# Performance work log

Hardware: AMD Instinct MI355X
Metric: run time of the kernel (lower is better)

## Reference

```python
import jax, jax.numpy as jnp
import numpy as np

T, B, S, E, H = 64, 64, 128, 512, 1024  # tgt_len, batch, src_len, emb, hidden


def setup_inputs() -> dict:
    key = jax.random.key(0)
    ks = jax.random.split(key, 14)
    s = 0.02  # weight init scale
    f32 = jnp.float32
    return {
        "inp": jax.random.normal(ks[0], (T, B, E), f32),
        "context": jax.random.normal(ks[1], (S, B, H), f32),
        "h0": jax.random.normal(ks[2], (2, B, H), f32) * 0.1,
        "c0": jax.random.normal(ks[3], (2, B, H), f32) * 0.1,
        # layer 0 LSTMCell: input = emb + input-feed = E + H
        "W_ih0": jax.random.normal(ks[4], (4 * H, E + H), f32) * s,
        "b_ih0": jnp.zeros((4 * H,), f32),
        "W_hh0": jax.random.normal(ks[5], (4 * H, H), f32) * s,
        "b_hh0": jnp.zeros((4 * H,), f32),
        # layer 1 LSTMCell: input = H
        "W_ih1": jax.random.normal(ks[6], (4 * H, H), f32) * s,
        "b_ih1": jnp.zeros((4 * H,), f32),
        "W_hh1": jax.random.normal(ks[7], (4 * H, H), f32) * s,
        "b_hh1": jnp.zeros((4 * H,), f32),
        # global attention (general): linear_in W_a (H,H), linear_out (H, 2H) no bias
        "W_a": jax.random.normal(ks[8], (H, H), f32) * s,
        "W_out": jax.random.normal(ks[9], (H, 2 * H), f32) * s,
    }


def _lstm_cell(x, h, c, W_ih, b_ih, W_hh, b_hh):
    # PyTorch gate order: i, f, g, o
    g = x @ W_ih.T + b_ih + h @ W_hh.T + b_hh
    i, f, gg, o = jnp.split(g, 4, axis=-1)
    c2 = jax.nn.sigmoid(f) * c + jax.nn.sigmoid(i) * jnp.tanh(gg)
    h2 = jax.nn.sigmoid(o) * jnp.tanh(c2)
    return h2, c2


def reference(inp, context, h0, c0, W_ih0, b_ih0, W_hh0, b_hh0,
              W_ih1, b_ih1, W_hh1, b_hh1, W_a, W_out):
    ctx_bt = jnp.transpose(context, (1, 0, 2))          # (B, S, H)
    # score(h, s) = h . (ctx_s @ W_a)  (== (h @ W_a.T) . ctx_s)
    ctx_p = jnp.einsum('bsk,kd->bsd', ctx_bt, W_a)      # (B, S, H)

    def step(carry, emb_t):
        h, c, out = carry                                # h,c: (2,B,H); out: (B,H)
        x = jnp.concatenate([emb_t, out], axis=1)        # (B, E+H) input feed
        h0n, c0n = _lstm_cell(x, h[0], c[0], W_ih0, b_ih0, W_hh0, b_hh0)
        h1n, c1n = _lstm_cell(h0n, h[1], c[1], W_ih1, b_ih1, W_hh1, b_hh1)
        score = jnp.einsum('bh,bsh->bs', h1n, ctx_p)     # (B, S)
        align = jax.nn.softmax(score, axis=-1)
        cvec = jnp.einsum('bs,bsh->bh', align, ctx_bt)   # (B, H)
        attn_h = jnp.tanh(jnp.concatenate([cvec, h1n], axis=1) @ W_out.T)
        hn = jnp.stack([h0n, h1n])
        cn = jnp.stack([c0n, c1n])
        return (hn, cn, attn_h), (attn_h, align)

    out0 = jnp.zeros((context.shape[1], W_a.shape[0]), context.dtype)
    (hF, cF, _), (outs, attns) = jax.lax.scan(step, (h0, c0, out0), inp)
    # outs: (T, B, H); hF, cF: (2, B, H); attns: (T, B, S)
    return outs, hF, cF, attns
```

## Files before the change

### kernel.cpp

```cpp
#include <hip/hip_runtime.h>

#define T_ 64
#define B_ 64
#define S_ 128
#define E_ 512
#define H_ 1024
#define BH (B_ * H_)

#define W0ROW (E_ + 2 * H_ + 8)
#define W1ROW (2 * H_ + 8)
#define SMEM_BYTES ((16 * W0ROW + 16 * W1ROW) * 2)

typedef __attribute__((ext_vector_type(8))) short short8;
typedef __attribute__((ext_vector_type(4))) short short4v;
typedef __attribute__((ext_vector_type(4))) float f32x4;

static __device__ __forceinline__ float bf2f(ushort u) {
  union { float f; unsigned u; } x; x.u = ((unsigned)u) << 16; return x.f;
}
static __device__ __forceinline__ ushort f2bf(float f) {
  union { float f; unsigned u; } x; x.f = f;
  unsigned r = 0x7FFFu + ((x.u >> 16) & 1u);
  return (ushort)((x.u + r) >> 16);
}
static __device__ __forceinline__ float sigm(float x) {
  return 1.f / (1.f + expf(-x));
}

static __device__ __forceinline__ void st32_dev(unsigned* p, unsigned v) {
  __hip_atomic_store(p, v, __ATOMIC_RELAXED, __HIP_MEMORY_SCOPE_AGENT);
}
static __device__ __forceinline__ unsigned ld32_dev(const unsigned* p) {
  return __hip_atomic_load(p, __ATOMIC_RELAXED, __HIP_MEMORY_SCOPE_AGENT);
}
static __device__ __forceinline__ void stf_dev(float* p, float v) {
  union { float f; unsigned u; } x; x.f = v;
  st32_dev((unsigned*)p, x.u);
}

__global__ __launch_bounds__(256) void k_cvt(const float* __restrict__ src,
                                             ushort* __restrict__ dst, int n4) {
  int i = blockIdx.x * 256 + threadIdx.x;
  if (i >= n4) return;
  f32x4 v = ((const f32x4*)src)[i];
  short4v o;
  o[0] = (short)f2bf(v[0]); o[1] = (short)f2bf(v[1]);
  o[2] = (short)f2bf(v[2]); o[3] = (short)f2bf(v[3]);
  ((short4v*)dst)[i] = o;
}

__global__ __launch_bounds__(256) void k_cvtT(const float* __restrict__ src,
                                              ushort* __restrict__ dst) {
  __shared__ ushort tile[32][33];
  const int bx = blockIdx.x & 31;
  const int by = blockIdx.x >> 5;
  const int lx = threadIdx.x & 31, ly = threadIdx.x >> 5;
#pragma unroll
  for (int i = 0; i < 32; i += 8)
    tile[ly + i][lx] = f2bf(src[(size_t)(by * 32 + ly + i) * H_ + bx * 32 + lx]);
  __syncthreads();
#pragma unroll
  for (int i = 0; i < 32; i += 8)
    dst[(size_t)(bx * 32 + ly + i) * H_ + by * 32 + lx] = tile[lx][ly + i];
}

__global__ __launch_bounds__(256) void k_ctxp(const ushort* __restrict__ ctx,
                                              const ushort* __restrict__ WaT,
                                              ushort* __restrict__ ctxp) {
  const int tid = threadIdx.x;
  const int wave = tid >> 6, lane = tid & 63;
  const int quad = lane >> 4, l16 = lane & 15;
  const int m0 = blockIdx.x * 64 + wave * 16;
  const int n0 = blockIdx.y * 64;
  const ushort* ar = ctx + (size_t)(m0 + l16) * H_;
  const int koff = quad * 8;
  f32x4 acc[4] = {};
  for (int k0 = 0; k0 < H_; k0 += 32) {
    int kk = k0 + koff;
    short8 a = *(const short8*)(ar + kk);
#pragma unroll
    for (int nt = 0; nt < 4; ++nt) {
      short8 b = *(const short8*)(WaT + (size_t)(n0 + nt * 16 + l16) * H_ + kk);
      acc[nt] = __builtin_amdgcn_mfma_f32_16x16x32_bf16(a, b, acc[nt], 0, 0, 0);
    }
  }
#pragma unroll
  for (int nt = 0; nt < 4; ++nt)
#pragma unroll
    for (int r = 0; r < 4; ++r)
      ctxp[(size_t)(m0 + quad * 4 + r) * H_ + n0 + nt * 16 + l16] =
          f2bf(acc[nt][r]);
}

__global__ __launch_bounds__(256) void k_init(const float* __restrict__ h0in,
                                              ushort* __restrict__ h0b,
                                              ushort* __restrict__ h1b,
                                              ushort* __restrict__ fdb,
                                              unsigned* __restrict__ flags) {
  int i = blockIdx.x * 256 + threadIdx.x;
  h0b[i] = f2bf(h0in[i]);
  h1b[i] = f2bf(h0in[BH + i]);
  fdb[i] = 0;
  if (blockIdx.x == 0) flags[threadIdx.x * 16] = 0;
}

static __device__ __forceinline__ void grid_bar(unsigned* flags, unsigned gen) {
  __syncthreads();
  if (blockIdx.x == 0) {
    const int tid = threadIdx.x;
    if (tid > 0 && tid < 256) {
      while (ld32_dev(&flags[tid * 16]) < gen) __builtin_amdgcn_s_sleep(4);
    }
    __syncthreads();
    if (tid == 0) st32_dev(&flags[0], gen);
    __syncthreads();
  } else {
    if (threadIdx.x == 0) {
      st32_dev(&flags[blockIdx.x * 16], gen);
      while (ld32_dev(&flags[0]) < gen) __builtin_amdgcn_s_sleep(4);
    }
    __syncthreads();
  }
  asm volatile("" ::: "memory");
}

struct FusedP {
  const ushort* inp;
  const ushort* Wih0; const ushort* Whh0;
  const ushort* Wih1; const ushort* Whh1;
  const ushort* Wout;
  const ushort* ctx;
  const ushort* ctxp;
  const float* bih0; const float* bhh0;
  const float* bih1; const float* bhh1;
  const float* c0in;
  ushort* h0b;
  ushort* h1b;
  ushort* fdb;
  ushort* cvb;
  float* psb;
  float* outs; float* hF; float* cF; float* attns;
  unsigned* flags;
};

#define ST(w, r, c) ub[(w) * 272 + (r) * 17 + (c)]
#define RED(w, i)   ub[(w) * 256 + (i)]

__global__ __launch_bounds__(1024, 1) void k_fused(FusedP p) {
  extern __shared__ ushort wlds[];
  ushort* w0 = wlds;
  ushort* w1 = wlds + 16 * W0ROW;
  __shared__ float ub[2176];
  __shared__ float al[S_];
  const int blk = blockIdx.x;
  const int tid = threadIdx.x;
  const int wave = tid >> 6, lane = tid & 63;
  const int wg = wave & 3;
  const int kh = wave >> 2;
  const int quad = lane >> 4, l16 = lane & 15;
  const int j0 = blk * 4;

  for (int idx = tid; idx < 16 * 192; idx += 1024) {
    int r = idx / 192, c = (idx % 192) * 8;
    int n = (r >> 2) * H_ + j0 + (r & 3);
    *(short8*)(w0 + r * W0ROW + c) =
        *(const short8*)(p.Wih0 + (size_t)n * (E_ + H_) + c);
  }
  for (int idx = tid; idx < 16 * 128; idx += 1024) {
    int r = idx / 128, c = (idx % 128) * 8;
    int n = (r >> 2) * H_ + j0 + (r & 3);
    *(short8*)(w0 + r * W0ROW + (E_ + H_) + c) =
        *(const short8*)(p.Whh0 + (size_t)n * H_ + c);
  }
  for (int idx = tid; idx < 16 * 128; idx += 1024) {
    int r = idx / 128, c = (idx % 128) * 8;
    int n = (r >> 2) * H_ + j0 + (r & 3);
    *(short8*)(w1 + r * W1ROW + c) =
        *(const short8*)(p.Wih1 + (size_t)n * H_ + c);
  }
  for (int idx = tid; idx < 16 * 128; idx += 1024) {
    int r = idx / 128, c = (idx % 128) * 8;
    int n = (r >> 2) * H_ + j0 + (r & 3);
    *(short8*)(w1 + r * W1ROW + H_ + c) =
        *(const short8*)(p.Whh1 + (size_t)n * H_ + c);
  }
  __syncthreads();

  const int own_b = tid >> 2;
  const int own_jl = tid & 3;
  const int own_j = j0 + own_jl;
  const int own_idx = own_b * H_ + own_j;
  float c0reg = 0.f, c1reg = 0.f;
  float b0i = 0.f, b0f = 0.f, b0g = 0.f, b0o = 0.f;
  float b1i = 0.f, b1f = 0.f, b1g = 0.f, b1o = 0.f;
  if (tid < 256) {
    c0reg = p.c0in[own_idx];
    c1reg = p.c0in[BH + own_idx];
    b0i = p.bih0[own_j]          + p.bhh0[own_j];
    b0f = p.bih0[H_ + own_j]     + p.bhh0[H_ + own_j];
    b0g = p.bih0[2 * H_ + own_j] + p.bhh0[2 * H_ + own_j];
    b0o = p.bih0[3 * H_ + own_j] + p.bhh0[3 * H_ + own_j];
    b1i = p.bih1[own_j]          + p.bhh1[own_j];
    b1f = p.bih1[H_ + own_j]     + p.bhh1[H_ + own_j];
    b1g = p.bih1[2 * H_ + own_j] + p.bhh1[2 * H_ + own_j];
    b1o = p.bih1[3 * H_ + own_j] + p.bhh1[3 * H_ + own_j];
  }

  const ushort* w0r = w0 + l16 * W0ROW;
  const ushort* w1r = w1 + l16 * W1ROW;
  const int koff = quad * 8;

  const int b3 = blk >> 2, dq = blk & 3;
  const int d0 = dq * 256;

  unsigned gen = 0;

  for (int t = 0; t < T_; ++t) {
    const ushort* h0prev = p.h0b + (size_t)t * BH;
    ushort* h0new       = p.h0b + (size_t)(t + 1) * BH;
    const ushort* h1prev = p.h1b + (size_t)t * BH;
    ushort* h1new       = p.h1b + (size_t)(t + 1) * BH;
    const ushort* feedr  = p.fdb + (size_t)t * BH;
    ushort* feedw       = p.fdb + (size_t)(t + 1) * BH;
    ushort* cv          = p.cvb + (size_t)t * BH;
    float* pst          = p.psb + (size_t)t * B_ * S_ * 4;
    const int last = (t == T_ - 1);

    {
      const int arow = 16 * wg + l16;
      const ushort* er = p.inp + ((size_t)t * B_ + arow) * E_;
      const ushort* fr = feedr + (size_t)arow * H_;
      const ushort* hr = h0prev + (size_t)arow * H_;
      const int kbase = kh * 640;
      f32x4 acc = {};
#pragma unroll
      for (int k0 = 0; k0 < 640; k0 += 32) {
        int kk = kbase + k0 + koff;
        short8 a;
        if (kk < E_)            a = *(const short8*)(er + kk);
        else if (kk < E_ + H_)  a = *(const short8*)(fr + (kk - E_));
        else                    a = *(const short8*)(hr + (kk - E_ - H_));
        short8 b = *(const short8*)(w0r + kk);
        acc = __builtin_amdgcn_mfma_f32_16x16x32_bf16(a, b, acc, 0, 0, 0);
      }
      if (kh >= 2) {
#pragma unroll
        for (int r = 0; r < 4; ++r) ST(wave - 8, quad * 4 + r, l16) = acc[r];
      }
      __syncthreads();
      if (kh < 2) {
#pragma unroll
        for (int r = 0; r < 4; ++r) {
          float s = ST(wave, quad * 4 + r, l16) + acc[r];
          ST(wave, quad * 4 + r, l16) = s;
        }
      }
      __syncthreads();
      if (tid < 256) {
        const int w = own_b >> 4, bl = own_b & 15;
        float gi = ST(w, bl, 0 + own_jl)  + ST(w + 4, bl, 0 + own_jl)  + b0i;
        float gf = ST(w, bl, 4 + own_jl)  + ST(w + 4, bl, 4 + own_jl)  + b0f;
        float gg = ST(w, bl, 8 + own_jl)  + ST(w + 4, bl, 8 + own_jl)  + b0g;
        float go = ST(w, bl, 12 + own_jl) + ST(w + 4, bl, 12 + own_jl) + b0o;
        float cn = sigm(gf) * c0reg + sigm(gi) * tanhf(gg);
        float hn = sigm(go) * tanhf(cn);
        c0reg = cn;
        if (last) { p.hF[own_idx] = hn; p.cF[own_idx] = cn; }
        unsigned u = f2bf(hn);
        unsigned up = __shfl_down(u, 1);
        if (!(own_jl & 1))
          st32_dev((unsigned*)h0new + own_b * (H_ / 2) + blk * 2 + (own_jl >> 1),
                   u | (up << 16));
      }
    }
    grid_bar(p.flags, ++gen);

    {
      const int arow = 16 * wg + l16;
      const ushort* xr = h0new + (size_t)arow * H_;
      const ushort* hr = h1prev + (size_t)arow * H_;
      const int kbase = kh * 512;
      f32x4 acc = {};
#pragma unroll
      for (int k0 = 0; k0 < 512; k0 += 32) {
        int kk = kbase + k0 + koff;
        short8 a = (kk < H_) ? *(const short8*)(xr + kk)
                             : *(const short8*)(hr + (kk - H_));
        short8 b = *(const short8*)(w1r + kk);
        acc = __builtin_amdgcn_mfma_f32_16x16x32_bf16(a, b, acc, 0, 0, 0);
      }
      if (kh >= 2) {
#pragma unroll
        for (int r = 0; r < 4; ++r) ST(wave - 8, quad * 4 + r, l16) = acc[r];
      }
      __syncthreads();
      if (kh < 2) {
#pragma unroll
        for (int r = 0; r < 4; ++r) {
          float s = ST(wave, quad * 4 + r, l16) + acc[r];
          ST(wave, quad * 4 + r, l16) = s;
        }
      }
      __syncthreads();
      if (tid < 256) {
        const int w = own_b >> 4, bl = own_b & 15;
        float gi = ST(w, bl, 0 + own_jl)  + ST(w + 4, bl, 0 + own_jl)  + b1i;
        float gf = ST(w, bl, 4 + own_jl)  + ST(w + 4, bl, 4 + own_jl)  + b1f;
        float gg = ST(w, bl, 8 + own_jl)  + ST(w + 4, bl, 8 + own_jl)  + b1g;
        float go = ST(w, bl, 12 + own_jl) + ST(w + 4, bl, 12 + own_jl) + b1o;
        float cn = sigm(gf) * c1reg + sigm(gi) * tanhf(gg);
        float hn = sigm(go) * tanhf(cn);
        c1reg = cn;
        if (last) { p.hF[BH + own_idx] = hn; p.cF[BH + own_idx] = cn; }
        unsigned u = f2bf(hn);
        unsigned up = __shfl_down(u, 1);
        if (!(own_jl & 1))
          st32_dev((unsigned*)h1new + own_b * (H_ / 2) + blk * 2 + (own_jl >> 1),
                   u | (up << 16));
      }
    }
    grid_bar(p.flags, ++gen);

    {
      short4v qv = *(const short4v*)(h1new + (size_t)b3 * H_ + d0 + lane * 4);
      float q0 = bf2f((ushort)qv[0]), q1 = bf2f((ushort)qv[1]);
      float q2 = bf2f((ushort)qv[2]), q3 = bf2f((ushort)qv[3]);
#pragma unroll
      for (int i = 0; i < 8; ++i) {
        const int s = wave * 8 + i;
        short4v v = *(const short4v*)(p.ctxp + ((size_t)s * B_ + b3) * H_ +
                                      d0 + lane * 4);
        float pr = bf2f((ushort)v[0]) * q0 + bf2f((ushort)v[1]) * q1 +
                   bf2f((ushort)v[2]) * q2 + bf2f((ushort)v[3]) * q3;
#pragma unroll
        for (int off = 32; off; off >>= 1) pr += __shfl_down(pr, off);
        if (lane == 0) stf_dev(pst + (b3 * S_ + s) * 4 + dq, pr);
      }
    }
    grid_bar(p.flags, ++gen);

    {
      if (tid < S_) {
        f32x4 ps = *(const f32x4*)(pst + (b3 * S_ + tid) * 4);
        al[tid] = ps[0] + ps[1] + ps[2] + ps[3];
      }
      __syncthreads();
      if (wave == 0) {
        float m = fmaxf(al[lane], al[lane + 64]);
#pragma unroll
        for (int off = 32; off; off >>= 1) m = fmaxf(m, __shfl_down(m, off));
        m = __shfl(m, 0);
        float e0 = expf(al[lane] - m), e1 = expf(al[lane + 64] - m);
        float s2 = e0 + e1;
#pragma unroll
        for (int off = 32; off; off >>= 1) s2 += __shfl_down(s2, off);
        s2 = __shfl(s2, 0);
        float inv = 1.f / s2;
        al[lane] = e0 * inv;
        al[lane + 64] = e1 * inv;
      }
      __syncthreads();
      if (dq == 0 && tid < S_)
        p.attns[((size_t)t * B_ + b3) * S_ + tid] = al[tid];
      float a0 = 0.f, a1 = 0.f, a2 = 0.f, a3 = 0.f;
#pragma unroll
      for (int i = 0; i < 8; ++i) {
        const int s = wave * 8 + i;
        short4v v = *(const short4v*)(p.ctx + ((size_t)s * B_ + b3) * H_ +
                                      d0 + lane * 4);
        float w = al[s];
        a0 += w * bf2f((ushort)v[0]);
        a1 += w * bf2f((ushort)v[1]);
        a2 += w * bf2f((ushort)v[2]);
        a3 += w * bf2f((ushort)v[3]);
      }
      __syncthreads();
      if (wave >= 8) {
        RED(wave - 8, lane * 4 + 0) = a0;
        RED(wave - 8, lane * 4 + 1) = a1;
        RED(wave - 8, lane * 4 + 2) = a2;
        RED(wave - 8, lane * 4 + 3) = a3;
      }
      __syncthreads();
      if (wave < 8) {
        RED(wave, lane * 4 + 0) += a0;
        RED(wave, lane * 4 + 1) += a1;
        RED(wave, lane * 4 + 2) += a2;
        RED(wave, lane * 4 + 3) += a3;
      }
      __syncthreads();
      if (tid < 256) {
        float val = 0.f;
#pragma unroll
        for (int w = 0; w < 8; ++w) val += RED(w, tid);
        unsigned u = f2bf(val);
        unsigned up = __shfl_down(u, 1);
        if (!(tid & 1))
          st32_dev((unsigned*)cv + (b3 * H_ + d0 + tid) / 2, u | (up << 16));
      }
    }
    grid_bar(p.flags, ++gen);

    if (blk < 64) {
      const int pj0 = blk * 16;
      const int arow = 16 * wg + l16;
      const ushort* cr = cv + (size_t)arow * H_;
      const ushort* hr2 = h1new + (size_t)arow * H_;
      const ushort* wr = p.Wout + (size_t)(pj0 + l16) * (2 * H_);
      const int kbase = kh * 512;
      f32x4 acc = {};
#pragma unroll
      for (int k0 = 0; k0 < 512; k0 += 32) {
        int kk = kbase + k0 + koff;
        short8 a = (kk < H_) ? *(const short8*)(cr + kk)
                             : *(const short8*)(hr2 + (kk - H_));
        short8 b = *(const short8*)(wr + kk);
        acc = __builtin_amdgcn_mfma_f32_16x16x32_bf16(a, b, acc, 0, 0, 0);
      }
      if (kh >= 2) {
#pragma unroll
        for (int r = 0; r < 4; ++r) ST(wave - 8, quad * 4 + r, l16) = acc[r];
      }
      __syncthreads();
      if (kh < 2) {
#pragma unroll
        for (int r = 0; r < 4; ++r) {
          float s = ST(wave, quad * 4 + r, l16) + acc[r];
          ST(wave, quad * 4 + r, l16) = s;
        }
      }
      __syncthreads();
      {
        const int b = tid >> 4;
        const int jl = tid & 15;
        const int w = b >> 4, bl = b & 15;
        float v = tanhf(ST(w, bl, jl) + ST(w + 4, bl, jl));
        p.outs[(size_t)t * B_ * H_ + b * H_ + pj0 + jl] = v;
        unsigned u = f2bf(v);
        unsigned up = __shfl_down(u, 1);
        if (!(jl & 1))
          st32_dev((unsigned*)feedw + b * (H_ / 2) + blk * 8 + (jl >> 1),
                   u | (up << 16));
      }
    }
    grid_bar(p.flags, ++gen);
  }
}

extern "C" void kernel_launch(void* const* d_in, const int* in_sizes, int n_in,
                              void* d_out, int out_size, void* d_ws, size_t ws_size,
                              hipStream_t stream) {
  const float* inpf  = (const float*)d_in[0];
  const float* ctxf  = (const float*)d_in[1];
  const float* h0in  = (const float*)d_in[2];
  const float* c0in  = (const float*)d_in[3];
  const float* Wih0f = (const float*)d_in[4];
  const float* bih0  = (const float*)d_in[5];
  const float* Whh0f = (const float*)d_in[6];
  const float* bhh0  = (const float*)d_in[7];
  const float* Wih1f = (const float*)d_in[8];
  const float* bih1  = (const float*)d_in[9];
  const float* Whh1f = (const float*)d_in[10];
  const float* bhh1  = (const float*)d_in[11];
  const float* Waf   = (const float*)d_in[12];
  const float* Woutf = (const float*)d_in[13];

  float* out = (float*)d_out;
  float* outs  = out;
  float* hF    = out + (size_t)T_ * B_ * H_;
  float* cF    = hF + 2 * BH;
  float* attns = cF + 2 * BH;

  char* p = (char*)d_ws;
  auto take = [&](size_t bytes) -> char* {
    char* q = p;
    p += (bytes + 255) & ~(size_t)255;
    return q;
  };
  ushort* h0b  = (ushort*)take((size_t)(T_ + 1) * BH * 2);
  ushort* h1b  = (ushort*)take((size_t)(T_ + 1) * BH * 2);
  ushort* fdb  = (ushort*)take((size_t)(T_ + 1) * BH * 2);
  ushort* cvb  = (ushort*)take((size_t)T_ * BH * 2);
  float* psb   = (float*)take((size_t)T_ * B_ * S_ * 4 * 4);
  unsigned* flags = (unsigned*)take(256 * 16 * sizeof(unsigned));
  ushort* WaT  = (ushort*)take((size_t)H_ * H_ * 2);
  ushort* ctxp = (ushort*)take((size_t)S_ * B_ * H_ * 2);

  struct { const float* src; int n; } cv[7] = {
    {Wih0f, 4 * H_ * (E_ + H_)}, {Whh0f, 4 * H_ * H_},
    {Wih1f, 4 * H_ * H_},        {Whh1f, 4 * H_ * H_},
    {Woutf, 2 * H_ * H_},
    {inpf,  T_ * B_ * E_},       {ctxf,  S_ * B_ * H_},
  };
  ushort* cb[7];
  for (int i = 0; i < 7; ++i) {
    cb[i] = (ushort*)take((size_t)cv[i].n * 2);
    int n4 = cv[i].n / 4;
    k_cvt<<<(n4 + 255) / 256, 256, 0, stream>>>(cv[i].src, cb[i], n4);
  }
  const ushort *Wih0 = cb[0], *Whh0 = cb[1], *Wih1 = cb[2], *Whh1 = cb[3],
               *Wout = cb[4], *inp = cb[5], *ctx = cb[6];

  k_cvtT<<<(H_ / 32) * (H_ / 32), 256, 0, stream>>>(Waf, WaT);
  k_ctxp<<<dim3((S_ * B_) / 64, H_ / 64), 256, 0, stream>>>(ctx, WaT, ctxp);
  k_init<<<BH / 256, 256, 0, stream>>>(h0in, h0b, h1b, fdb, flags);

  static int smem_set = 0;
  if (!smem_set) {
    hipFuncSetAttribute((const void*)k_fused,
                        hipFuncAttributeMaxDynamicSharedMemorySize, SMEM_BYTES);
    smem_set = 1;
  }

  FusedP fp;
  fp.inp = inp; fp.Wih0 = Wih0; fp.Whh0 = Whh0; fp.Wih1 = Wih1; fp.Whh1 = Whh1;
  fp.Wout = Wout; fp.ctx = ctx; fp.ctxp = ctxp;
  fp.bih0 = bih0; fp.bhh0 = bhh0; fp.bih1 = bih1; fp.bhh1 = bhh1;
  fp.c0in = c0in;
  fp.h0b = h0b; fp.h1b = h1b; fp.fdb = fdb; fp.cvb = cvb; fp.psb = psb;
  fp.outs = outs; fp.hF = hF; fp.cF = cF; fp.attns = attns;
  fp.flags = flags;
  void* kargs[] = {(void*)&fp};
  hipLaunchCooperativeKernel(k_fused, dim3(256), dim3(1024), kargs,
                             (unsigned)SMEM_BYTES, stream);
}
```

Before: 3.567 ms.

## Precompute context@Wout and replace two grid barriers with per-batch counters

```diff
diff --git a/kernel.cpp b/kernel.cpp
--- a/kernel.cpp
+++ b/kernel.cpp
@@ -36,6 +36,9 @@
 static __device__ __forceinline__ void stf_dev(float* p, float v) {
   union { float f; unsigned u; } x; x.f = v;
   st32_dev((unsigned*)p, x.u);
+}
+static __device__ __forceinline__ void add_dev(unsigned* p) {
+  __hip_atomic_fetch_add(p, 1u, __ATOMIC_RELAXED, __HIP_MEMORY_SCOPE_AGENT);
 }
 
 __global__ __launch_bounds__(256) void k_cvt(const float* __restrict__ src,
@@ -47,6 +50,11 @@
   o[0] = (short)f2bf(v[0]); o[1] = (short)f2bf(v[1]);
   o[2] = (short)f2bf(v[2]); o[3] = (short)f2bf(v[3]);
   ((short4v*)dst)[i] = o;
+}
+
+__global__ __launch_bounds__(256) void k_zero(unsigned* __restrict__ p, int n) {
+  int i = blockIdx.x * 256 + threadIdx.x;
+  if (i < n) p[i] = 0;
 }
 
 __global__ __launch_bounds__(256) void k_cvtT(const float* __restrict__ src,
@@ -92,6 +100,35 @@
           f2bf(acc[nt][r]);
 }
 
+__global__ __launch_bounds__(256) void k_ctxo(const ushort* __restrict__ ctx,
+                                              const ushort* __restrict__ Wout,
+                                              ushort* __restrict__ ctxo) {
+  const int tid = threadIdx.x;
+  const int wave = tid >> 6, lane = tid & 63;
+  const int quad = lane >> 4, l16 = lane & 15;
+  const int m0 = blockIdx.x * 64 + wave * 16;
+  const int n0 = blockIdx.y * 64;
+  const ushort* ar = ctx + (size_t)(m0 + l16) * H_;
+  const int koff = quad * 8;
+  f32x4 acc[4] = {};
+  for (int k0 = 0; k0 < H_; k0 += 32) {
+    int kk = k0 + koff;
+    short8 a = *(const short8*)(ar + kk);
+#pragma unroll
+    for (int nt = 0; nt < 4; ++nt) {
+      short8 b = *(const short8*)(Wout +
+                                  (size_t)(n0 + nt * 16 + l16) * (2 * H_) + kk);
+      acc[nt] = __builtin_amdgcn_mfma_f32_16x16x32_bf16(a, b, acc[nt], 0, 0, 0);
+    }
+  }
+#pragma unroll
+  for (int nt = 0; nt < 4; ++nt)
+#pragma unroll
+    for (int r = 0; r < 4; ++r)
+      ctxo[(size_t)(m0 + quad * 4 + r) * H_ + n0 + nt * 16 + l16] =
+          f2bf(acc[nt][r]);
+}
+
 __global__ __launch_bounds__(256) void k_init(const float* __restrict__ h0in,
                                               ushort* __restrict__ h0b,
                                               ushort* __restrict__ h1b,
@@ -129,16 +166,18 @@
   const ushort* Wih0; const ushort* Whh0;
   const ushort* Wih1; const ushort* Whh1;
   const ushort* Wout;
-  const ushort* ctx;
   const ushort* ctxp;
+  const ushort* ctxo;
   const float* bih0; const float* bhh0;
   const float* bih1; const float* bhh1;
   const float* c0in;
   ushort* h0b;
   ushort* h1b;
   ushort* fdb;
-  ushort* cvb;
   float* psb;
+  float* gemmb;
+  unsigned* done;
+  unsigned* gdone;
   float* outs; float* hF; float* cF; float* attns;
   unsigned* flags;
 };
@@ -222,8 +261,8 @@
     ushort* h1new       = p.h1b + (size_t)(t + 1) * BH;
     const ushort* feedr  = p.fdb + (size_t)t * BH;
     ushort* feedw       = p.fdb + (size_t)(t + 1) * BH;
-    ushort* cv          = p.cvb + (size_t)t * BH;
     float* pst          = p.psb + (size_t)t * B_ * S_ * 4;
+    float* gemm_t       = p.gemmb + (size_t)t * BH;
     const int last = (t == T_ - 1);
 
     {
@@ -336,10 +375,56 @@
         for (int off = 32; off; off >>= 1) pr += __shfl_down(pr, off);
         if (lane == 0) stf_dev(pst + (b3 * S_ + s) * 4 + dq, pr);
       }
-    }
-    grid_bar(p.flags, ++gen);
+      if (blk < 64) {
+        const int pj0 = blk * 16;
+        const int arow = 16 * wg + l16;
+        const ushort* hr2 = h1new + (size_t)arow * H_;
+        const ushort* wr = p.Wout + (size_t)(pj0 + l16) * (2 * H_) + H_;
+        const int kbase = kh * 256;
+        f32x4 acc = {};
+#pragma unroll
+        for (int k0 = 0; k0 < 256; k0 += 32) {
+          int kk = kbase + k0 + koff;
+          acc = __builtin_amdgcn_mfma_f32_16x16x32_bf16(
+              *(const short8*)(hr2 + kk), *(const short8*)(wr + kk), acc,
+              0, 0, 0);
+        }
+        if (kh >= 2) {
+#pragma unroll
+          for (int r = 0; r < 4; ++r) ST(wave - 8, quad * 4 + r, l16) = acc[r];
+        }
+        __syncthreads();
+        if (kh < 2) {
+#pragma unroll
+          for (int r = 0; r < 4; ++r) {
+            float s = ST(wave, quad * 4 + r, l16) + acc[r];
+            ST(wave, quad * 4 + r, l16) = s;
+          }
+        }
+        __syncthreads();
+        {
+          const int b = tid >> 4;
+          const int jl = tid & 15;
+          const int w = b >> 4, bl = b & 15;
+          stf_dev(gemm_t + b * H_ + pj0 + jl,
+                  ST(w, bl, jl) + ST(w + 4, bl, jl));
+        }
+      }
+      __syncthreads();
+      if (tid == 0) {
+        add_dev(p.done + (((unsigned)(t << 6) + b3) << 4));
+        if (blk < 64) add_dev(p.gdone + (((unsigned)(t << 2) + (blk >> 4)) << 4));
+      }
+    }
 
     {
+      if (tid == 0) {
+        const unsigned* dp = p.done + (((unsigned)(t << 6) + b3) << 4);
+        while (ld32_dev(dp) < 4) __builtin_amdgcn_s_sleep(2);
+        const unsigned* gp = p.gdone + (((unsigned)(t << 2) + dq) << 4);
+        while (ld32_dev(gp) < 16) __builtin_amdgcn_s_sleep(2);
+      }
+      __syncthreads();
       if (tid < S_) {
         f32x4 ps = *(const f32x4*)(pst + (b3 * S_ + tid) * 4);
         al[tid] = ps[0] + ps[1] + ps[2] + ps[3];
@@ -362,85 +447,28 @@
       __syncthreads();
       if (dq == 0 && tid < S_)
         p.attns[((size_t)t * B_ + b3) * S_ + tid] = al[tid];
-      float a0 = 0.f, a1 = 0.f, a2 = 0.f, a3 = 0.f;
-#pragma unroll
-      for (int i = 0; i < 8; ++i) {
-        const int s = wave * 8 + i;
-        short4v v = *(const short4v*)(p.ctx + ((size_t)s * B_ + b3) * H_ +
-                                      d0 + lane * 4);
-        float w = al[s];
-        a0 += w * bf2f((ushort)v[0]);
-        a1 += w * bf2f((ushort)v[1]);
-        a2 += w * bf2f((ushort)v[2]);
-        a3 += w * bf2f((ushort)v[3]);
-      }
-      __syncthreads();
-      if (wave >= 8) {
-        RED(wave - 8, lane * 4 + 0) = a0;
-        RED(wave - 8, lane * 4 + 1) = a1;
-        RED(wave - 8, lane * 4 + 2) = a2;
-        RED(wave - 8, lane * 4 + 3) = a3;
-      }
-      __syncthreads();
-      if (wave < 8) {
-        RED(wave, lane * 4 + 0) += a0;
-        RED(wave, lane * 4 + 1) += a1;
-        RED(wave, lane * 4 + 2) += a2;
-        RED(wave, lane * 4 + 3) += a3;
+      {
+        const int sg = tid >> 8, jj = tid & 255;
+        const ushort* cop = p.ctxo + (size_t)b3 * H_ + d0 + jj;
+        float a0 = 0.f;
+#pragma unroll
+        for (int i = 0; i < 32; ++i) {
+          int s = sg * 32 + i;
+          a0 += al[s] * bf2f(cop[(size_t)s * B_ * H_]);
+        }
+        RED(sg, jj) = a0;
       }
       __syncthreads();
       if (tid < 256) {
-        float val = 0.f;
-#pragma unroll
-        for (int w = 0; w < 8; ++w) val += RED(w, tid);
-        unsigned u = f2bf(val);
-        unsigned up = __shfl_down(u, 1);
-        if (!(tid & 1))
-          st32_dev((unsigned*)cv + (b3 * H_ + d0 + tid) / 2, u | (up << 16));
-      }
-    }
-    grid_bar(p.flags, ++gen);
-
-    if (blk < 64) {
-      const int pj0 = blk * 16;
-      const int arow = 16 * wg + l16;
-      const ushort* cr = cv + (size_t)arow * H_;
-      const ushort* hr2 = h1new + (size_t)arow * H_;
-      const ushort* wr = p.Wout + (size_t)(pj0 + l16) * (2 * H_);
-      const int kbase = kh * 512;
-      f32x4 acc = {};
-#pragma unroll
-      for (int k0 = 0; k0 < 512; k0 += 32) {
-        int kk = kbase + k0 + koff;
-        short8 a = (kk < H_) ? *(const short8*)(cr + kk)
-                             : *(const short8*)(hr2 + (kk - H_));
-        short8 b = *(const short8*)(wr + kk);
-        acc = __builtin_amdgcn_mfma_f32_16x16x32_bf16(a, b, acc, 0, 0, 0);
-      }
-      if (kh >= 2) {
-#pragma unroll
-        for (int r = 0; r < 4; ++r) ST(wave - 8, quad * 4 + r, l16) = acc[r];
-      }
-      __syncthreads();
-      if (kh < 2) {
-#pragma unroll
-        for (int r = 0; r < 4; ++r) {
-          float s = ST(wave, quad * 4 + r, l16) + acc[r];
-          ST(wave, quad * 4 + r, l16) = s;
-        }
-      }
-      __syncthreads();
-      {
-        const int b = tid >> 4;
-        const int jl = tid & 15;
-        const int w = b >> 4, bl = b & 15;
-        float v = tanhf(ST(w, bl, jl) + ST(w + 4, bl, jl));
-        p.outs[(size_t)t * B_ * H_ + b * H_ + pj0 + jl] = v;
+        const int jj = tid;
+        float val = RED(0, jj) + RED(1, jj) + RED(2, jj) + RED(3, jj) +
+                    gemm_t[b3 * H_ + d0 + jj];
+        float v = tanhf(val);
+        p.outs[(size_t)t * B_ * H_ + b3 * H_ + d0 + jj] = v;
         unsigned u = f2bf(v);
         unsigned up = __shfl_down(u, 1);
-        if (!(jl & 1))
-          st32_dev((unsigned*)feedw + b * (H_ / 2) + blk * 8 + (jl >> 1),
-                   u | (up << 16));
+        if (!(jj & 1))
+          st32_dev((unsigned*)feedw + (b3 * H_ + d0 + jj) / 2, u | (up << 16));
       }
     }
     grid_bar(p.flags, ++gen);
@@ -480,11 +508,14 @@
   ushort* h0b  = (ushort*)take((size_t)(T_ + 1) * BH * 2);
   ushort* h1b  = (ushort*)take((size_t)(T_ + 1) * BH * 2);
   ushort* fdb  = (ushort*)take((size_t)(T_ + 1) * BH * 2);
-  ushort* cvb  = (ushort*)take((size_t)T_ * BH * 2);
   float* psb   = (float*)take((size_t)T_ * B_ * S_ * 4 * 4);
+  float* gemmb = (float*)take((size_t)T_ * BH * 4);
+  unsigned* done  = (unsigned*)take((size_t)T_ * 64 * 16 * 4);
+  unsigned* gdone = (unsigned*)take((size_t)T_ * 4 * 16 * 4);
   unsigned* flags = (unsigned*)take(256 * 16 * sizeof(unsigned));
   ushort* WaT  = (ushort*)take((size_t)H_ * H_ * 2);
   ushort* ctxp = (ushort*)take((size_t)S_ * B_ * H_ * 2);
+  ushort* ctxo = (ushort*)take((size_t)S_ * B_ * H_ * 2);
 
   struct { const float* src; int n; } cv[7] = {
     {Wih0f, 4 * H_ * (E_ + H_)}, {Whh0f, 4 * H_ * H_},
@@ -503,6 +534,11 @@
 
   k_cvtT<<<(H_ / 32) * (H_ / 32), 256, 0, stream>>>(Waf, WaT);
   k_ctxp<<<dim3((S_ * B_) / 64, H_ / 64), 256, 0, stream>>>(ctx, WaT, ctxp);
+  k_ctxo<<<dim3((S_ * B_) / 64, H_ / 64), 256, 0, stream>>>(ctx, Wout, ctxo);
+  {
+    int nz = T_ * 64 * 16 + T_ * 4 * 16;
+    k_zero<<<(nz + 255) / 256, 256, 0, stream>>>(done, nz);
+  }
   k_init<<<BH / 256, 256, 0, stream>>>(h0in, h0b, h1b, fdb, flags);
 
   static int smem_set = 0;
@@ -514,10 +550,11 @@
 
   FusedP fp;
   fp.inp = inp; fp.Wih0 = Wih0; fp.Whh0 = Whh0; fp.Wih1 = Wih1; fp.Whh1 = Whh1;
-  fp.Wout = Wout; fp.ctx = ctx; fp.ctxp = ctxp;
+  fp.Wout = Wout; fp.ctxp = ctxp; fp.ctxo = ctxo;
   fp.bih0 = bih0; fp.bhh0 = bhh0; fp.bih1 = bih1; fp.bhh1 = bhh1;
   fp.c0in = c0in;
-  fp.h0b = h0b; fp.h1b = h1b; fp.fdb = fdb; fp.cvb = cvb; fp.psb = psb;
+  fp.h0b = h0b; fp.h1b = h1b; fp.fdb = fdb; fp.psb = psb; fp.gemmb = gemmb;
+  fp.done = done; fp.gdone = gdone;
   fp.outs = outs; fp.hF = hF; fp.cF = cF; fp.attns = attns;
   fp.flags = flags;
   void* kargs[] = {(void*)&fp};
```

Result: slower. 3.876 ms (+8.7%).
